# Optimization experiments

Hardware: AMD Instinct MI355X
Metric: run time of the kernel (lower is better)

The kernel has to match this reference:

```python
import jax, jax.numpy as jnp
import numpy as np

N = 100000   # nodes
E = 1600000  # edges (avg degree 16)
D = 128      # feature dim (in_dim = out_dim = 128)


def setup_inputs() -> dict:
    key = jax.random.key(0)
    k0, k1, k2, k3, k4, k5 = jax.random.split(key, 6)
    x = jax.random.normal(k0, (N, D), dtype=jnp.float32)
    edge_index = jax.random.randint(k1, (2, E), 0, N, dtype=jnp.int32)
    # GCNConv linear weights (PyG stores lin.weight [out,in]; math is x @ W.T, here W:[in,out])
    s1 = 1.0 / np.sqrt(D)
    W1 = jax.random.uniform(k2, (D, D), jnp.float32, -s1, s1)
    b1 = jnp.zeros((D,), jnp.float32)
    W2 = jax.random.uniform(k3, (D, D), jnp.float32, -s1, s1)
    b2 = jnp.zeros((D,), jnp.float32)
    return {"x": x, "edge_index": edge_index, "W1": W1, "b1": b1, "W2": W2, "b2": b2}


def reference(x, edge_index, W1, b1, W2, b2):
    n = x.shape[0]
    idt = edge_index.dtype
    loop = jnp.arange(n, dtype=idt)
    src = jnp.concatenate([edge_index[0], loop])  # message sources
    dst = jnp.concatenate([edge_index[1], loop])  # aggregation targets
    # improved=True -> self-loop fill value 2.0; edge_weight=None -> ones
    w = jnp.concatenate([jnp.ones((edge_index.shape[1],), x.dtype),
                         jnp.full((n,), 2.0, x.dtype)])
    deg = jax.ops.segment_sum(w, dst, num_segments=n)
    dinv = jnp.where(deg > 0, jax.lax.rsqrt(deg), 0.0)
    norm = dinv[src] * w * dinv[dst]  # [E+N] symmetric GCN normalization

    def conv(h, W, b):
        h = h @ W  # [N, D] dense transform
        agg = jax.ops.segment_sum(norm[:, None] * h[src], dst, num_segments=n)
        return agg + b

    h = conv(x, W1, b1)        # conv1
    for _ in range(4):
        h = conv(h, W2, b2)
    return h
```

## Files before the change

### kernel.cpp

```cpp
#include <hip/hip_runtime.h>
#include <hip/hip_fp16.h>

#define D 128

typedef _Float16 half8 __attribute__((ext_vector_type(8)));
typedef float floatx4 __attribute__((ext_vector_type(4)));


__device__ inline void acc_h4(float& ax, float& ay, float& az, float& aw,
                              float w, uint2 raw) {
    __half2 h01 = *reinterpret_cast<const __half2*>(&raw.x);
    __half2 h23 = *reinterpret_cast<const __half2*>(&raw.y);
    ax = fmaf(w, __low2float(h01), ax);
    ay = fmaf(w, __high2float(h01), ay);
    az = fmaf(w, __low2float(h23), az);
    aw = fmaf(w, __high2float(h23), aw);
}


__global__ void k_zero(int* __restrict__ p, int n) {
    int i = blockIdx.x * 256 + threadIdx.x;
    if (i < n) p[i] = 0;
}

__global__ void k_count(const int* __restrict__ dst, int* __restrict__ cnt,
                        int* __restrict__ rank, int e) {
    int i = blockIdx.x * 256 + threadIdx.x;
    if (i < e) rank[i] = atomicAdd(&cnt[dst[i]], 1);
}

__global__ void k_f2h(const float* __restrict__ in, __half* __restrict__ out, int n8) {
    int i = blockIdx.x * 256 + threadIdx.x;
    if (i < n8) {
        const float4* p = (const float4*)in + (size_t)i * 2;
        float4 a = p[0], b = p[1];
        __half2 h0 = __float22half2_rn(make_float2(a.x, a.y));
        __half2 h1 = __float22half2_rn(make_float2(a.z, a.w));
        __half2 h2 = __float22half2_rn(make_float2(b.x, b.y));
        __half2 h3 = __float22half2_rn(make_float2(b.z, b.w));
        uint4 o;
        o.x = *(unsigned*)&h0; o.y = *(unsigned*)&h1;
        o.z = *(unsigned*)&h2; o.w = *(unsigned*)&h3;
        ((uint4*)out)[i] = o;
    }
}


__global__ __launch_bounds__(256) void k_scanA(const int* __restrict__ cnt,
                                               int* __restrict__ partials,
                                               float* __restrict__ dinv, int n) {
    __shared__ int s[256];
    int b = blockIdx.x, t = threadIdx.x;
    int i0 = b * 512 + t * 2;
    int v = 0;
    if (i0 < n) {
        int c0 = cnt[i0];
        v += c0;
        dinv[i0] = 1.0f / sqrtf((float)(c0 + 2));
    }
    if (i0 + 1 < n) {
        int c1 = cnt[i0 + 1];
        v += c1;
        dinv[i0 + 1] = 1.0f / sqrtf((float)(c1 + 2));
    }
    s[t] = v;
    __syncthreads();
    for (int off = 128; off > 0; off >>= 1) {
        if (t < off) s[t] += s[t + off];
        __syncthreads();
    }
    if (t == 0) partials[b] = s[0];
}

__global__ __launch_bounds__(512) void k_scanB(const int* __restrict__ partials,
                                               int* __restrict__ base,
                                               int* __restrict__ off_n, int nb) {
    __shared__ int s[512];
    int t = threadIdx.x;
    int v = (t < nb) ? partials[t] : 0;
    s[t] = v;
    __syncthreads();
    for (int off = 1; off < 512; off <<= 1) {
        int x = (t >= off) ? s[t - off] : 0;
        __syncthreads();
        s[t] += x;
        __syncthreads();
    }
    if (t < nb) base[t] = s[t] - v;
    if (t == nb - 1) off_n[0] = s[t];
}

__global__ __launch_bounds__(256) void k_scanC(const int* __restrict__ cnt,
                                               const int* __restrict__ base,
                                               int* __restrict__ offsets, int n) {
    __shared__ int s[256];
    int b = blockIdx.x, t = threadIdx.x;
    int i0 = b * 512 + t * 2;
    int v0 = (i0 < n) ? cnt[i0] : 0;
    int v1 = (i0 + 1 < n) ? cnt[i0 + 1] : 0;
    int sum = v0 + v1;
    s[t] = sum;
    __syncthreads();
    for (int off = 1; off < 256; off <<= 1) {
        int x = (t >= off) ? s[t - off] : 0;
        __syncthreads();
        s[t] += x;
        __syncthreads();
    }
    int excl = s[t] - sum + base[b];
    if (i0 < n) offsets[i0] = excl;
    if (i0 + 1 < n) offsets[i0 + 1] = excl + v0;
}

__global__ void k_fill(const int* __restrict__ src, const int* __restrict__ dst,
                       const int* __restrict__ rank, const int* __restrict__ offsets,
                       const float* __restrict__ dinv, int2* __restrict__ csr, int e) {
    int i = blockIdx.x * 256 + threadIdx.x;
    if (i < e) {
        int s = src[i];
        int d = dst[i];
        int pos = offsets[d] + rank[i];
        csr[pos] = make_int2(s, __float_as_int(dinv[s] * dinv[d]));
    }
}

__global__ __launch_bounds__(128) void k_wmm(const float* __restrict__ A,
                                             const float* __restrict__ B,
                                             float* __restrict__ Cm) {
    __shared__ float a[128];
    int r = blockIdx.x, d = threadIdx.x;
    a[d] = A[r * 128 + d];
    __syncthreads();
    float acc = 0.0f;
#pragma unroll 8
    for (int k = 0; k < 128; k++) acc += a[k] * B[k * 128 + d];
    Cm[r * 128 + d] = acc;
}

__global__ __launch_bounds__(128) void k_wmm_bias(const float* __restrict__ W1,
                                                  const float* __restrict__ W4,
                                                  const float* __restrict__ W2,
                                                  const float* __restrict__ b1,
                                                  const float* __restrict__ b2,
                                                  __half* __restrict__ pack,
                                                  float* __restrict__ cmat) {
    __shared__ float s[128];
    int d = threadIdx.x;
    if (blockIdx.x < 128) {
        int r = blockIdx.x;
        s[d] = W1[r * 128 + d];
        __syncthreads();
        float acc = 0.0f;
#pragma unroll 8
        for (int k = 0; k < 128; k++) acc += s[k] * W4[k * 128 + d];
        int ss = r >> 5, j = r & 7;
        int l = ((r >> 3) & 3) * 16 + (d & 15);
        int t = d >> 4;
        int tid = ss * 512 + t * 64 + l;
        __half hh = __float2half(acc);
        float rem = acc - __half2float(hh);
        pack[(size_t)tid * 8 + j] = hh;
        pack[16384 + (size_t)tid * 8 + j] = __float2half(rem);
        return;
    }
    float v = b2[d];
    cmat[d] = v;
    for (int j = 1; j <= 3; j++) {
        s[d] = v;
        __syncthreads();
        float acc = 0.0f;
#pragma unroll 8
        for (int k = 0; k < 128; k++) acc += s[k] * W2[k * 128 + d];
        v = acc;
        cmat[j * 128 + d] = v;
        __syncthreads();
    }
    s[d] = b1[d];
    __syncthreads();
    float acc = 0.0f;
#pragma unroll 8
    for (int k = 0; k < 128; k++) acc += s[k] * W4[k * 128 + d];
    cmat[4 * 128 + d] = acc;
}

__global__ __launch_bounds__(256) void k_matmul(const __half* __restrict__ Hh,
                                                const __half* __restrict__ Wpack,
                                                float* __restrict__ O,
                                                const float* __restrict__ ucol,
                                                const float* __restrict__ cmat,
                                                int nrows) {
    const int t = threadIdx.x;
    const int lane = t & 63, wave = t >> 6;
    const int rows0 = blockIdx.x * 64 + wave * 16;
    const int lrow = lane & 15, lk = lane >> 4;

    float uu[4][4];
#pragma unroll
    for (int r = 0; r < 4; r++) {
        int row = rows0 + lk * 4 + r;
        if (row >= nrows) row = nrows - 1;
#pragma unroll
        for (int tt = 0; tt < 4; tt++) uu[tt][r] = ucol[(size_t)tt * nrows + row];
    }

    floatx4 acc[8];
#pragma unroll
    for (int tl = 0; tl < 8; tl++) {
        int col = tl * 16 + lrow;
        float c0 = cmat[col];
        float c1 = cmat[128 + col], c2 = cmat[256 + col];
        float c3 = cmat[384 + col], c4 = cmat[512 + col];
#pragma unroll
        for (int r = 0; r < 4; r++)
            acc[tl][r] = c0 + uu[0][r] * c1 + uu[1][r] * c2
                            + uu[2][r] * c3 + uu[3][r] * c4;
    }

    int arow = rows0 + lrow;
    if (arow >= nrows) arow = nrows - 1;
    const __half* abase = Hh + (size_t)arow * 128 + lk * 8;

#pragma unroll
    for (int s = 0; s < 4; s++) {
        half8 a = *reinterpret_cast<const half8*>(abase + s * 32);
        const __half* wb = Wpack + (size_t)s * 4096 + (size_t)lane * 8;
#pragma unroll
        for (int tl = 0; tl < 8; tl++) {
            half8 bh = *reinterpret_cast<const half8*>(wb + (size_t)tl * 512);
            half8 bl = *reinterpret_cast<const half8*>(wb + (size_t)tl * 512 + 16384);
            acc[tl] = __builtin_amdgcn_mfma_f32_16x16x32_f16(a, bh, acc[tl], 0, 0, 0);
            acc[tl] = __builtin_amdgcn_mfma_f32_16x16x32_f16(a, bl, acc[tl], 0, 0, 0);
        }
    }

#pragma unroll
    for (int r = 0; r < 4; r++) {
        int row = rows0 + lk * 4 + r;
        if (row < nrows) {
            float* orow = O + (size_t)row * 128 + lrow;
#pragma unroll
            for (int tl = 0; tl < 8; tl++) orow[tl * 16] = acc[tl][r];
        }
    }
}

template <bool WITH_U, bool IN_F16, bool OUT_F16>
__global__ __launch_bounds__(256) void k_gather(const void* __restrict__ Tv,
                                                const int2* __restrict__ csr,
                                                const int* __restrict__ offsets,
                                                const float* __restrict__ dinv,
                                                void* __restrict__ Ov,
                                                const float* __restrict__ uin,
                                                float* __restrict__ uout, int n) {
    int node = blockIdx.x * 4 + (threadIdx.x >> 6);
    if (node >= n) return;
    int lane = threadIdx.x & 63;
    int hf = lane >> 5;
    int c = (lane & 31) << 2;
    const __half* Tch = (const __half*)Tv + c;
    const float*  Tcf = (const float*)Tv + c;

    float ax = 0.f, ay = 0.f, az = 0.f, aw = 0.f;
    float uacc = 0.f;
    if (hf == 0) {
        float di = dinv[node];
        float sw = 2.0f * di * di;
        if (IN_F16) {
            uint2 raw = *(const uint2*)(Tch + (size_t)node * D);
            acc_h4(ax, ay, az, aw, sw, raw);
        } else {
            float4 v = *(const float4*)(Tcf + (size_t)node * D);
            ax = sw * v.x; ay = sw * v.y; az = sw * v.z; aw = sw * v.w;
        }
        if (WITH_U) uacc = sw * (uin ? uin[node] : 1.0f);
    }

    int e = offsets[node];
    const int e1 = offsets[node + 1];

    for (; e + 8 <= e1; e += 8) {
        int2 p0 = csr[e + hf];
        int2 p1 = csr[e + 2 + hf];
        int2 p2 = csr[e + 4 + hf];
        int2 p3 = csr[e + 6 + hf];
        float w0 = __int_as_float(p0.y), w1 = __int_as_float(p1.y);
        float w2 = __int_as_float(p2.y), w3 = __int_as_float(p3.y);
        if (IN_F16) {
            uint2 r0 = *(const uint2*)(Tch + (size_t)p0.x * D);
            uint2 r1 = *(const uint2*)(Tch + (size_t)p1.x * D);
            uint2 r2 = *(const uint2*)(Tch + (size_t)p2.x * D);
            uint2 r3 = *(const uint2*)(Tch + (size_t)p3.x * D);
            if (WITH_U) {
                if (uin) {
                    uacc += w0 * uin[p0.x] + w1 * uin[p1.x]
                          + w2 * uin[p2.x] + w3 * uin[p3.x];
                } else {
                    uacc += w0 + w1 + w2 + w3;
                }
            }
            acc_h4(ax, ay, az, aw, w0, r0);
            acc_h4(ax, ay, az, aw, w1, r1);
            acc_h4(ax, ay, az, aw, w2, r2);
            acc_h4(ax, ay, az, aw, w3, r3);
        } else {
            float4 v0 = *(const float4*)(Tcf + (size_t)p0.x * D);
            float4 v1 = *(const float4*)(Tcf + (size_t)p1.x * D);
            float4 v2 = *(const float4*)(Tcf + (size_t)p2.x * D);
            float4 v3 = *(const float4*)(Tcf + (size_t)p3.x * D);
            if (WITH_U) {
                if (uin) {
                    uacc += w0 * uin[p0.x] + w1 * uin[p1.x]
                          + w2 * uin[p2.x] + w3 * uin[p3.x];
                } else {
                    uacc += w0 + w1 + w2 + w3;
                }
            }
            ax += w0 * v0.x; ay += w0 * v0.y; az += w0 * v0.z; aw += w0 * v0.w;
            ax += w1 * v1.x; ay += w1 * v1.y; az += w1 * v1.z; aw += w1 * v1.w;
            ax += w2 * v2.x; ay += w2 * v2.y; az += w2 * v2.z; aw += w2 * v2.w;
            ax += w3 * v3.x; ay += w3 * v3.y; az += w3 * v3.z; aw += w3 * v3.w;
        }
    }
    for (; e + 2 <= e1; e += 2) {
        int2 p0 = csr[e + hf];
        float w0 = __int_as_float(p0.y);
        if (WITH_U) uacc += w0 * (uin ? uin[p0.x] : 1.0f);
        if (IN_F16) {
            uint2 r0 = *(const uint2*)(Tch + (size_t)p0.x * D);
            acc_h4(ax, ay, az, aw, w0, r0);
        } else {
            float4 v0 = *(const float4*)(Tcf + (size_t)p0.x * D);
            ax += w0 * v0.x; ay += w0 * v0.y; az += w0 * v0.z; aw += w0 * v0.w;
        }
    }
    if (e < e1 && hf == 0) {
        int2 p0 = csr[e];
        float w0 = __int_as_float(p0.y);
        if (WITH_U) uacc += w0 * (uin ? uin[p0.x] : 1.0f);
        if (IN_F16) {
            uint2 r0 = *(const uint2*)(Tch + (size_t)p0.x * D);
            acc_h4(ax, ay, az, aw, w0, r0);
        } else {
            float4 v0 = *(const float4*)(Tcf + (size_t)p0.x * D);
            ax += w0 * v0.x; ay += w0 * v0.y; az += w0 * v0.z; aw += w0 * v0.w;
        }
    }

    ax += __shfl_xor(ax, 32, 64);
    ay += __shfl_xor(ay, 32, 64);
    az += __shfl_xor(az, 32, 64);
    aw += __shfl_xor(aw, 32, 64);
    if (WITH_U) uacc += __shfl_xor(uacc, 32, 64);

    if (hf == 0) {
        if (OUT_F16) {
            __half2 o01 = __float22half2_rn(make_float2(ax, ay));
            __half2 o23 = __float22half2_rn(make_float2(az, aw));
            float2 raw;
            *(__half2*)&raw.x = o01;
            *(__half2*)&raw.y = o23;
            *(float2*)((__half*)Ov + (size_t)node * D + c) = raw;
        } else {
            *(float4*)((float*)Ov + (size_t)node * D + c) =
                make_float4(ax, ay, az, aw);
        }
        if (WITH_U && lane == 0) uout[node] = uacc;
    }
}


extern "C" void kernel_launch(void* const* d_in, const int* in_sizes, int n_in,
                              void* d_out, int out_size, void* d_ws, size_t ws_size,
                              hipStream_t stream) {
    const float* x  = (const float*)d_in[0];
    const int*   ei = (const int*)d_in[1];
    const float* W1 = (const float*)d_in[2];
    const float* b1 = (const float*)d_in[3];
    const float* W2 = (const float*)d_in[4];
    const float* b2 = (const float*)d_in[5];
    const int N = in_sizes[0] / D;
    const int E = in_sizes[1] / 2;
    float* out = (float*)d_out;

    char* ws = (char*)d_ws;
    size_t woff = 0;
    auto alloc = [&](size_t bytes) -> void* {
        void* p = ws + woff;
        woff = (woff + bytes + 15) & ~(size_t)15;
        return p;
    };
    __half* T16a    = (__half*)alloc((size_t)N * D * sizeof(__half));
    __half* T16b    = (__half*)alloc((size_t)N * D * sizeof(__half));
    int*   cnt      = (int*)  alloc((size_t)N * sizeof(int));
    int*   offsets  = (int*)  alloc((size_t)(N + 1) * sizeof(int));
    int*   rank     = (int*)  alloc((size_t)E * sizeof(int));
    float* dinv     = (float*)alloc((size_t)N * sizeof(float));
    int2*  csr      = (int2*) alloc((size_t)E * sizeof(int2));
    int*   partials = (int*)  alloc(1024 * sizeof(int));
    int*   base     = (int*)  alloc(1024 * sizeof(int));
    float* ucol     = (float*)alloc((size_t)4 * N * sizeof(float));
    float* cmat     = (float*)alloc(5 * 128 * sizeof(float));
    float* Wsq      = (float*)alloc(128 * 128 * sizeof(float));
    float* W4       = (float*)alloc(128 * 128 * sizeof(float));
    __half* Wpack   = (__half*)alloc(32768 * sizeof(__half));
    size_t x16_bytes = (size_t)N * D * sizeof(__half);
    bool use_x16 = (woff + x16_bytes) <= ws_size;
    __half* X16 = use_x16 ? (__half*)alloc(x16_bytes) : nullptr;
    (void)n_in; (void)out_size;

    const int* e_src = ei;
    const int* e_dst = ei + E;
    const int NB = (N + 511) / 512;

    k_zero<<<(N + 255) / 256, 256, 0, stream>>>(cnt, N);
    k_count<<<(E + 255) / 256, 256, 0, stream>>>(e_dst, cnt, rank, E);
    k_scanA<<<NB, 256, 0, stream>>>(cnt, partials, dinv, N);
    k_scanB<<<1, 512, 0, stream>>>(partials, base, offsets + N, NB);
    k_scanC<<<NB, 256, 0, stream>>>(cnt, base, offsets, N);
    k_fill<<<(E + 255) / 256, 256, 0, stream>>>(e_src, e_dst, rank, offsets,
                                                dinv, csr, E);

    const int GG = (N + 3) / 4;
    if (use_x16) {
        int n8 = (N * D) / 8;
        k_f2h<<<(n8 + 255) / 256, 256, 0, stream>>>(x, X16, n8);
        k_gather<true, true, true><<<GG, 256, 0, stream>>>(
            X16, csr, offsets, dinv, T16a, nullptr, ucol, N);
    } else {
        k_gather<true, false, true><<<GG, 256, 0, stream>>>(
            x, csr, offsets, dinv, T16a, nullptr, ucol, N);
    }
    k_gather<true,  true, true><<<GG, 256, 0, stream>>>(
        T16a, csr, offsets, dinv, T16b, ucol,         ucol + N,     N);
    k_gather<true,  true, true><<<GG, 256, 0, stream>>>(
        T16b, csr, offsets, dinv, T16a, ucol + N,     ucol + 2 * N, N);
    k_gather<true,  true, true><<<GG, 256, 0, stream>>>(
        T16a, csr, offsets, dinv, T16b, ucol + 2 * N, ucol + 3 * N, N);
    k_gather<false, true, true><<<GG, 256, 0, stream>>>(
        T16b, csr, offsets, dinv, T16a, nullptr,      nullptr,      N);

    k_wmm<<<128, 128, 0, stream>>>(W2, W2, Wsq);
    k_wmm<<<128, 128, 0, stream>>>(Wsq, Wsq, W4);
    k_wmm_bias<<<129, 128, 0, stream>>>(W1, W4, W2, b1, b2, Wpack, cmat);

    k_matmul<<<(N + 63) / 64, 256, 0, stream>>>(T16a, Wpack, out, ucol, cmat, N);
}
```

Baseline: 662.1 us.

## Fuse final gather with dense matmul epilogue into single kernel

The last aggregation pass and the final MFMA matmul are merged: each 4-node block aggregates its rows into shared memory, then its waves compute the output via MFMA with only 4 of 16 rows populated. This removes writing and re-reading the last fp16 intermediate and one kernel launch. In exchange MFMA utilization drops to a quarter, Wpack is reloaded per 4-node block, and the weight precompute kernels are moved to the start of the launch sequence.

New measurement: 715.2 us. +8.0%, slower.

```diff
diff --git a/kernel.cpp b/kernel.cpp
--- a/kernel.cpp
+++ b/kernel.cpp
@@ -183,73 +183,12 @@
     cmat[4 * 128 + d] = acc;
 }
 
-__global__ __launch_bounds__(256) void k_matmul(const __half* __restrict__ Hh,
-                                                const __half* __restrict__ Wpack,
-                                                float* __restrict__ O,
-                                                const float* __restrict__ ucol,
-                                                const float* __restrict__ cmat,
-                                                int nrows) {
-    const int t = threadIdx.x;
-    const int lane = t & 63, wave = t >> 6;
-    const int rows0 = blockIdx.x * 64 + wave * 16;
-    const int lrow = lane & 15, lk = lane >> 4;
-
-    float uu[4][4];
-#pragma unroll
-    for (int r = 0; r < 4; r++) {
-        int row = rows0 + lk * 4 + r;
-        if (row >= nrows) row = nrows - 1;
-#pragma unroll
-        for (int tt = 0; tt < 4; tt++) uu[tt][r] = ucol[(size_t)tt * nrows + row];
-    }
-
-    floatx4 acc[8];
-#pragma unroll
-    for (int tl = 0; tl < 8; tl++) {
-        int col = tl * 16 + lrow;
-        float c0 = cmat[col];
-        float c1 = cmat[128 + col], c2 = cmat[256 + col];
-        float c3 = cmat[384 + col], c4 = cmat[512 + col];
-#pragma unroll
-        for (int r = 0; r < 4; r++)
-            acc[tl][r] = c0 + uu[0][r] * c1 + uu[1][r] * c2
-                            + uu[2][r] * c3 + uu[3][r] * c4;
-    }
-
-    int arow = rows0 + lrow;
-    if (arow >= nrows) arow = nrows - 1;
-    const __half* abase = Hh + (size_t)arow * 128 + lk * 8;
-
-#pragma unroll
-    for (int s = 0; s < 4; s++) {
-        half8 a = *reinterpret_cast<const half8*>(abase + s * 32);
-        const __half* wb = Wpack + (size_t)s * 4096 + (size_t)lane * 8;
-#pragma unroll
-        for (int tl = 0; tl < 8; tl++) {
-            half8 bh = *reinterpret_cast<const half8*>(wb + (size_t)tl * 512);
-            half8 bl = *reinterpret_cast<const half8*>(wb + (size_t)tl * 512 + 16384);
-            acc[tl] = __builtin_amdgcn_mfma_f32_16x16x32_f16(a, bh, acc[tl], 0, 0, 0);
-            acc[tl] = __builtin_amdgcn_mfma_f32_16x16x32_f16(a, bl, acc[tl], 0, 0, 0);
-        }
-    }
-
-#pragma unroll
-    for (int r = 0; r < 4; r++) {
-        int row = rows0 + lk * 4 + r;
-        if (row < nrows) {
-            float* orow = O + (size_t)row * 128 + lrow;
-#pragma unroll
-            for (int tl = 0; tl < 8; tl++) orow[tl * 16] = acc[tl][r];
-        }
-    }
-}
-
-template <bool WITH_U, bool IN_F16, bool OUT_F16>
+template <bool WITH_U, bool IN_F16>
 __global__ __launch_bounds__(256) void k_gather(const void* __restrict__ Tv,
                                                 const int2* __restrict__ csr,
                                                 const int* __restrict__ offsets,
                                                 const float* __restrict__ dinv,
-                                                void* __restrict__ Ov,
+                                                __half* __restrict__ Ov,
                                                 const float* __restrict__ uin,
                                                 float* __restrict__ uout, int n) {
     int node = blockIdx.x * 4 + (threadIdx.x >> 6);
@@ -353,18 +292,142 @@
     if (WITH_U) uacc += __shfl_xor(uacc, 32, 64);
 
     if (hf == 0) {
-        if (OUT_F16) {
-            __half2 o01 = __float22half2_rn(make_float2(ax, ay));
-            __half2 o23 = __float22half2_rn(make_float2(az, aw));
-            float2 raw;
-            *(__half2*)&raw.x = o01;
-            *(__half2*)&raw.y = o23;
-            *(float2*)((__half*)Ov + (size_t)node * D + c) = raw;
+        __half2 o01 = __float22half2_rn(make_float2(ax, ay));
+        __half2 o23 = __float22half2_rn(make_float2(az, aw));
+        float2 raw;
+        *(__half2*)&raw.x = o01;
+        *(__half2*)&raw.y = o23;
+        *(float2*)(Ov + (size_t)node * D + c) = raw;
+        if (WITH_U && lane == 0) uout[node] = uacc;
+    }
+}
+
+__global__ __launch_bounds__(256) void k_gather_mm(const __half* __restrict__ Tv,
+                                                   const int2* __restrict__ csr,
+                                                   const int* __restrict__ offsets,
+                                                   const float* __restrict__ dinv,
+                                                   const __half* __restrict__ Wpack,
+                                                   float* __restrict__ O,
+                                                   const float* __restrict__ ucol,
+                                                   const float* __restrict__ cmat,
+                                                   int n) {
+    __shared__ __half rows[4][128];
+    const int wave = threadIdx.x >> 6;
+    const int lane = threadIdx.x & 63;
+    const int node0 = blockIdx.x * 4;
+    const int node = node0 + wave;
+    const bool active = node < n;
+
+    const int hf = lane >> 5;
+    const int c = (lane & 31) << 2;
+    const __half* Tch = Tv + c;
+
+    float ax = 0.f, ay = 0.f, az = 0.f, aw = 0.f;
+    if (active) {
+        if (hf == 0) {
+            float di = dinv[node];
+            float sw = 2.0f * di * di;
+            uint2 raw = *(const uint2*)(Tch + (size_t)node * D);
+            acc_h4(ax, ay, az, aw, sw, raw);
+        }
+        int e = offsets[node];
+        const int e1 = offsets[node + 1];
+        for (; e + 8 <= e1; e += 8) {
+            int2 p0 = csr[e + hf];
+            int2 p1 = csr[e + 2 + hf];
+            int2 p2 = csr[e + 4 + hf];
+            int2 p3 = csr[e + 6 + hf];
+            float w0 = __int_as_float(p0.y), w1 = __int_as_float(p1.y);
+            float w2 = __int_as_float(p2.y), w3 = __int_as_float(p3.y);
+            uint2 r0 = *(const uint2*)(Tch + (size_t)p0.x * D);
+            uint2 r1 = *(const uint2*)(Tch + (size_t)p1.x * D);
+            uint2 r2 = *(const uint2*)(Tch + (size_t)p2.x * D);
+            uint2 r3 = *(const uint2*)(Tch + (size_t)p3.x * D);
+            acc_h4(ax, ay, az, aw, w0, r0);
+            acc_h4(ax, ay, az, aw, w1, r1);
+            acc_h4(ax, ay, az, aw, w2, r2);
+            acc_h4(ax, ay, az, aw, w3, r3);
+        }
+        for (; e + 2 <= e1; e += 2) {
+            int2 p0 = csr[e + hf];
+            float w0 = __int_as_float(p0.y);
+            uint2 r0 = *(const uint2*)(Tch + (size_t)p0.x * D);
+            acc_h4(ax, ay, az, aw, w0, r0);
+        }
+        if (e < e1 && hf == 0) {
+            int2 p0 = csr[e];
+            float w0 = __int_as_float(p0.y);
+            uint2 r0 = *(const uint2*)(Tch + (size_t)p0.x * D);
+            acc_h4(ax, ay, az, aw, w0, r0);
+        }
+        ax += __shfl_xor(ax, 32, 64);
+        ay += __shfl_xor(ay, 32, 64);
+        az += __shfl_xor(az, 32, 64);
+        aw += __shfl_xor(aw, 32, 64);
+    }
+    if (hf == 0) {
+        __half2 o01 = __float22half2_rn(make_float2(ax, ay));
+        __half2 o23 = __float22half2_rn(make_float2(az, aw));
+        float2 raw;
+        *(__half2*)&raw.x = o01;
+        *(__half2*)&raw.y = o23;
+        if (!active) raw = make_float2(0.f, 0.f);
+        *(float2*)(&rows[wave][c]) = raw;
+    }
+    __syncthreads();
+
+    const int lrow = lane & 15, lk = lane >> 4;
+    const int t0 = 2 * wave;
+
+    floatx4 acc[2];
+#pragma unroll
+    for (int ti = 0; ti < 2; ti++) {
+        int col = (t0 + ti) * 16 + lrow;
+        float c0 = cmat[col];
+        float c1 = cmat[128 + col], c2 = cmat[256 + col];
+        float c3 = cmat[384 + col], c4 = cmat[512 + col];
+#pragma unroll
+        for (int r = 0; r < 4; r++) {
+            int rowN = node0 + lk * 4 + r;
+            float v = c0;
+            if (lk == 0 && rowN < n) {
+                v += ucol[(size_t)0 * n + rowN] * c1
+                   + ucol[(size_t)1 * n + rowN] * c2
+                   + ucol[(size_t)2 * n + rowN] * c3
+                   + ucol[(size_t)3 * n + rowN] * c4;
+            }
+            acc[ti][r] = v;
+        }
+    }
+
+#pragma unroll
+    for (int s = 0; s < 4; s++) {
+        half8 a;
+        if (lrow < 4) {
+            a = *reinterpret_cast<const half8*>(&rows[lrow][s * 32 + lk * 8]);
         } else {
-            *(float4*)((float*)Ov + (size_t)node * D + c) =
-                make_float4(ax, ay, az, aw);
-        }
-        if (WITH_U && lane == 0) uout[node] = uacc;
+            a = half8{0, 0, 0, 0, 0, 0, 0, 0};
+        }
+        const __half* wb = Wpack + (size_t)s * 4096 + (size_t)lane * 8;
+#pragma unroll
+        for (int ti = 0; ti < 2; ti++) {
+            half8 bh = *reinterpret_cast<const half8*>(wb + (size_t)(t0 + ti) * 512);
+            half8 bl = *reinterpret_cast<const half8*>(wb + (size_t)(t0 + ti) * 512 + 16384);
+            acc[ti] = __builtin_amdgcn_mfma_f32_16x16x32_f16(a, bh, acc[ti], 0, 0, 0);
+            acc[ti] = __builtin_amdgcn_mfma_f32_16x16x32_f16(a, bl, acc[ti], 0, 0, 0);
+        }
+    }
+
+    if (lk == 0) {
+#pragma unroll
+        for (int r = 0; r < 4; r++) {
+            int rowN = node0 + r;
+            if (rowN < n) {
+#pragma unroll
+                for (int ti = 0; ti < 2; ti++)
+                    O[(size_t)rowN * 128 + (t0 + ti) * 16 + lrow] = acc[ti][r];
+            }
+        }
     }
 }
 
@@ -412,6 +475,10 @@
     const int* e_dst = ei + E;
     const int NB = (N + 511) / 512;
 
+    k_wmm<<<128, 128, 0, stream>>>(W2, W2, Wsq);
+    k_wmm<<<128, 128, 0, stream>>>(Wsq, Wsq, W4);
+    k_wmm_bias<<<129, 128, 0, stream>>>(W1, W4, W2, b1, b2, Wpack, cmat);
+
     k_zero<<<(N + 255) / 256, 256, 0, stream>>>(cnt, N);
     k_count<<<(E + 255) / 256, 256, 0, stream>>>(e_dst, cnt, rank, E);
     k_scanA<<<NB, 256, 0, stream>>>(cnt, partials, dinv, N);
@@ -424,24 +491,18 @@
     if (use_x16) {
         int n8 = (N * D) / 8;
         k_f2h<<<(n8 + 255) / 256, 256, 0, stream>>>(x, X16, n8);
-        k_gather<true, true, true><<<GG, 256, 0, stream>>>(
+        k_gather<true, true><<<GG, 256, 0, stream>>>(
             X16, csr, offsets, dinv, T16a, nullptr, ucol, N);
     } else {
-        k_gather<true, false, true><<<GG, 256, 0, stream>>>(
+        k_gather<true, false><<<GG, 256, 0, stream>>>(
             x, csr, offsets, dinv, T16a, nullptr, ucol, N);
     }
-    k_gather<true,  true, true><<<GG, 256, 0, stream>>>(
+    k_gather<true, true><<<GG, 256, 0, stream>>>(
         T16a, csr, offsets, dinv, T16b, ucol,         ucol + N,     N);
-    k_gather<true,  true, true><<<GG, 256, 0, stream>>>(
+    k_gather<true, true><<<GG, 256, 0, stream>>>(
         T16b, csr, offsets, dinv, T16a, ucol + N,     ucol + 2 * N, N);
-    k_gather<true,  true, true><<<GG, 256, 0, stream>>>(
+    k_gather<true, true><<<GG, 256, 0, stream>>>(
         T16a, csr, offsets, dinv, T16b, ucol + 2 * N, ucol + 3 * N, N);
-    k_gather<false, true, true><<<GG, 256, 0, stream>>>(
-        T16b, csr, offsets, dinv, T16a, nullptr,      nullptr,      N);
-
-    k_wmm<<<128, 128, 0, stream>>>(W2, W2, Wsq);
-    k_wmm<<<128, 128, 0, stream>>>(Wsq, Wsq, W4);
-    k_wmm_bias<<<129, 128, 0, stream>>>(W1, W4, W2, b1, b2, Wpack, cmat);
-
-    k_matmul<<<(N + 63) / 64, 256, 0, stream>>>(T16a, Wpack, out, ucol, cmat, N);
-}
+    k_gather_mm<<<GG, 256, 0, stream>>>(
+        T16b, csr, offsets, dinv, Wpack, out, ucol, cmat, N);
+}
```
